# Optimization experiments

Hardware: AMD Instinct MI355X
Metric: run time of the kernel (lower is better)

## Reference

```python
import jax, jax.numpy as jnp
import numpy as np

FM = 128       # feature_maps
QM = 128       # query_maps
ROUNDS = 4     # test_rounds (training=False)
N_VARS = 24576
N_CLAUSES = 98304
N_EDGES = 3 * N_CLAUSES
EPS = 1e-6


def _dense(k, fan_in, fan_out):
    return jax.random.normal(k, (fan_in, fan_out), jnp.float32) * (1.0 / np.sqrt(fan_in))


def setup_inputs() -> dict:
    key = jax.random.key(0)
    ks = jax.random.split(key, 20)
    return {
        "edge_lit": jax.random.randint(ks[0], (N_EDGES,), 0, 2 * N_VARS, dtype=jnp.int32),
        "edge_clause": jnp.sort(jax.random.randint(ks[1], (N_EDGES,), 0, N_CLAUSES, dtype=jnp.int32)),
        "noise_v": jax.random.normal(ks[2], (ROUNDS, N_VARS, 4), jnp.float32),
        "noise_c": jax.random.normal(ks[3], (ROUNDS, N_CLAUSES, 4), jnp.float32),
        # variables_query: MLP(2, QM, QM), input FM+4
        "vq_w0": _dense(ks[4], FM + 4, QM), "vq_b0": jnp.zeros((QM,), jnp.float32),
        "vq_w1": _dense(ks[5], QM, QM),     "vq_b1": jnp.zeros((QM,), jnp.float32),
        # clauses_query: MLP(2, QM, QM), input FM+4
        "cq_w0": _dense(ks[6], FM + 4, QM), "cq_b0": jnp.zeros((QM,), jnp.float32),
        "cq_w1": _dense(ks[7], QM, QM),     "cq_b1": jnp.zeros((QM,), jnp.float32),
        # clause_update: MLP(2, 2*FM, FM+QM), input FM+2*QM=384
        "cm_w0": _dense(ks[8], FM + 2 * QM, 2 * FM), "cm_b0": jnp.zeros((2 * FM,), jnp.float32),
        "cm_w1": _dense(ks[9], 2 * FM, FM + QM),     "cm_b1": jnp.zeros((FM + QM,), jnp.float32),
        # update_gate: MLP(3, 2*FM, FM), input QM+FM+2*QM=512
        "ug_w0": _dense(ks[10], QM + FM + 2 * QM, 2 * FM), "ug_b0": jnp.zeros((2 * FM,), jnp.float32),
        "ug_w1": _dense(ks[11], 2 * FM, 2 * FM),           "ug_b1": jnp.zeros((2 * FM,), jnp.float32),
        "ug_w2": _dense(ks[12], 2 * FM, FM),               "ug_b2": jnp.zeros((FM,), jnp.float32),
        # clauses_mask_output: MLP(2, FM, 1)
        "co_w0": _dense(ks[13], FM, FM), "co_b0": jnp.zeros((FM,), jnp.float32),
        "co_w1": _dense(ks[14], FM, 1),  "co_b1": jnp.zeros((1,), jnp.float32),
        "n_vars": N_VARS,
        "n_clauses": N_CLAUSES,
    }


def _forward(edge_lit, edge_clause, n_vars, n_clauses, floats):
    (noise_v, noise_c,
     vq_w0, vq_b0, vq_w1, vq_b1,
     cq_w0, cq_b0, cq_w1, cq_b1,
     cm_w0, cm_b0, cm_w1, cm_b1,
     ug_w0, ug_b0, ug_w1, ug_b1, ug_w2, ug_b2,
     co_w0, co_b0, co_w1, co_b1) = floats

    n_edges = edge_lit.shape[0]
    # lit_degree = row sums of sparse adjacency (all nonzeros are 1.0)
    lit_degree = jax.ops.segment_sum(jnp.ones((n_edges,), jnp.float32), edge_lit,
                                     num_segments=2 * n_vars)[:, None]          # [2V,1]
    degree_weight = jax.lax.rsqrt(jnp.maximum(lit_degree, 1.0))
    var_degree_weight = 4.0 * jax.lax.rsqrt(
        jnp.maximum(lit_degree[:n_vars] + lit_degree[n_vars:], 1.0))            # [V,1]

    def mlp2(x, w0, b0, w1, b1):
        return jax.nn.relu(x @ w0 + b0) @ w1 + b1

    def mlp3(x, w0, b0, w1, b1, w2, b2):
        h = jax.nn.relu(x @ w0 + b0)
        h = jax.nn.relu(h @ w1 + b1)
        return h @ w2 + b2

    def pair_norm(x):
        # PairNorm(subtract_mean=True), single graph -> global mean over nodes
        x = x - jnp.mean(x, axis=0, keepdims=True)
        return x * jax.lax.rsqrt(jnp.mean(jnp.square(x)) + EPS)

    def clauses_loss_fn(vq, cq):
        # unsat_cnf_clauses_loss: softplus literal values aggregated per clause,
        # clause satisfiability exp(-sum), gated by clause query mask.
        lits = jax.nn.softplus(jnp.concatenate([vq, -vq], axis=0))              # [2V,Q]
        csum = jax.ops.segment_sum(lits[edge_lit], edge_clause,
                                   num_segments=n_clauses)                      # [C,Q]
        loss = jnp.exp(-csum) * jax.nn.sigmoid(cq)
        return jnp.mean(loss), loss

    grad_fn = jax.grad(clauses_loss_fn, argnums=(0, 1), has_aux=True)

    def step(carry, xs):
        variables, clauses = carry
        nv, nc = xs
        vq = mlp2(jnp.concatenate([variables, nv], -1), vq_w0, vq_b0, vq_w1, vq_b1)
        cq = mlp2(jnp.concatenate([clauses, nc], -1), cq_w0, cq_b0, cq_w1, cq_b1)
        (vgrad, cgrad), clauses_loss = grad_fn(vq, cq)
        vgrad = vgrad * var_degree_weight
        clauses_loss = clauses_loss * 4.0
        clause_data = mlp2(jnp.concatenate([clauses, clauses_loss, cgrad], -1),
                           cm_w0, cm_b0, cm_w1, cm_b1)                          # [C,FM+QM]
        variables_loss_all = clause_data[:, :QM]
        clauses = pair_norm(clause_data[:, QM:]) * 0.25 + 0.1 * clauses
        # adj_matrix @ variables_loss_all (literal-side aggregation)
        variables_loss = jax.ops.segment_sum(variables_loss_all[edge_clause], edge_lit,
                                             num_segments=2 * n_vars) * degree_weight
        unit = jnp.concatenate([vgrad, variables,
                                variables_loss[:n_vars], variables_loss[n_vars:]], -1)
        variables = pair_norm(mlp3(unit, ug_w0, ug_b0, ug_w1, ug_b1, ug_w2, ug_b2)) * 0.25 \
                    + 0.1 * variables
        logits = mlp2(clauses, co_w0, co_b0, co_w1, co_b1)[:, 0]                # [C]
        return (variables, clauses), logits

    init = (jnp.ones((n_vars, FM), jnp.float32), jnp.ones((n_clauses, FM), jnp.float32))
    _, logits = jax.lax.scan(step, init, (noise_v, noise_c))                    # [R,C]
    return jax.nn.sigmoid(logits), jax.nn.softplus(logits)


def reference(edge_lit, edge_clause, noise_v, noise_c,
              vq_w0, vq_b0, vq_w1, vq_b1,
              cq_w0, cq_b0, cq_w1, cq_b1,
              cm_w0, cm_b0, cm_w1, cm_b1,
              ug_w0, ug_b0, ug_w1, ug_b1, ug_w2, ug_b2,
              co_w0, co_b0, co_w1, co_b1,
              n_vars, n_clauses):
    floats = (noise_v, noise_c,
              vq_w0, vq_b0, vq_w1, vq_b1,
              cq_w0, cq_b0, cq_w1, cq_b1,
              cm_w0, cm_b0, cm_w1, cm_b1,
              ug_w0, ug_b0, ug_w1, ug_b1, ug_w2, ug_b2,
              co_w0, co_b0, co_w1, co_b1)
    return _forward(edge_lit, edge_clause, int(n_vars), int(n_clauses), floats)
```

## Files before the change

### kernel.cpp

```cpp
#include <hip/hip_runtime.h>
#include <math.h>

#define NV 24576
#define NC 98304
#define NE 294912
#define CMCHUNK 24576

typedef unsigned short bf16;
using bf8 = __attribute__((ext_vector_type(8))) short;
using f4  = __attribute__((ext_vector_type(4))) float;

static constexpr float INV_CQM = 1.0f / 12582912.0f;
static constexpr float LOG2E = 1.44269504f;
static constexpr float LN2 = 0.69314718f;

__device__ __forceinline__ float b2f(bf16 h) { return __uint_as_float(((unsigned)h) << 16); }
__device__ __forceinline__ bf16 f2b(float f) {
  unsigned u = __float_as_uint(f);
  u += 0x7fff + ((u >> 16) & 1);
  return (bf16)(u >> 16);
}
__device__ __forceinline__ float fexp2(float x) { float r; asm("v_exp_f32 %0, %1" : "=v"(r) : "v"(x)); return r; }
__device__ __forceinline__ float flog2(float x) { float r; asm("v_log_f32 %0, %1" : "=v"(r) : "v"(x)); return r; }
__device__ __forceinline__ float frcpf(float x) { float r; asm("v_rcp_f32 %0, %1" : "=v"(r) : "v"(x)); return r; }
__device__ __forceinline__ float fsigm(float x) { return frcpf(1.0f + fexp2(-x * LOG2E)); }
__device__ __forceinline__ float fsoftplus(float x) {
  return fmaxf(x, 0.0f) + LN2 * flog2(1.0f + fexp2(-fabsf(x) * LOG2E));
}
__device__ __forceinline__ float cvt_ld(float x) { return x; }
__device__ __forceinline__ float cvt_ld(bf16 x) { return b2f(x); }

__device__ __forceinline__ void gload16(const void* g, void* l) {
  __builtin_amdgcn_global_load_lds((const __attribute__((address_space(1))) unsigned int*)g,
                                   (__attribute__((address_space(3))) unsigned int*)l, 16, 0, 0);
}


__global__ __launch_bounds__(256) void k_cptr(const int* __restrict__ ec, int* __restrict__ ptr) {
  int c = blockIdx.x * 256 + threadIdx.x;
  if (c > NC) return;
  int lo = 0, hi = NE;
  while (lo < hi) { int mid = (lo + hi) >> 1; if (ec[mid] < c) lo = mid + 1; else hi = mid; }
  ptr[c] = lo;
}

__global__ __launch_bounds__(256) void k_litcnt(const int* __restrict__ el, int* __restrict__ cnt) {
  int e = blockIdx.x * 256 + threadIdx.x;
  atomicAdd(&cnt[el[e]], 1);
}

__global__ __launch_bounds__(1024) void k_scan(int* __restrict__ cnt, int* __restrict__ ptr) {
  __shared__ int wsum[16];
  __shared__ int carry_s;
  int tid = threadIdx.x, lane = tid & 63, w = tid >> 6;
  if (tid == 0) carry_s = 0;
  __syncthreads();
  for (int base = 0; base < 2 * NV; base += 1024) {
    int x = cnt[base + tid];
    int v = x;
#pragma unroll
    for (int off = 1; off < 64; off <<= 1) {
      int y = __shfl_up(v, off, 64);
      if (lane >= off) v += y;
    }
    if (lane == 63) wsum[w] = v;
    __syncthreads();
    int carry = carry_s;
    int wpre = 0;
    for (int i = 0; i < w; ++i) wpre += wsum[i];
    int excl = carry + wpre + (v - x);
    ptr[base + tid] = excl;
    cnt[base + tid] = excl;
    __syncthreads();
    if (tid == 1023) carry_s = carry + wpre + v;
  }
  __syncthreads();
  if (tid == 0) ptr[2 * NV] = carry_s;
}

__global__ __launch_bounds__(256) void k_fillsort(const int* __restrict__ el, const int* __restrict__ ec,
                                                  int* __restrict__ cur, int* __restrict__ lclause) {
  int e = blockIdx.x * 256 + threadIdx.x;
  int pos = atomicAdd(&cur[el[e]], 1);
  lclause[pos] = ec[e];
}

__global__ __launch_bounds__(256) void k_degree(const int* __restrict__ lptr, float* __restrict__ dw,
                                                float* __restrict__ vdw) {
  int l = blockIdx.x * 256 + threadIdx.x;
  if (l < 2 * NV) dw[l] = rsqrtf(fmaxf((float)(lptr[l + 1] - lptr[l]), 1.0f));
  if (l < NV) {
    int d = (lptr[l + 1] - lptr[l]) + (lptr[l + NV + 1] - lptr[l + NV]);
    vdw[l] = 4.0f * rsqrtf(fmaxf((float)d, 1.0f));
  }
}

__global__ __launch_bounds__(256) void k_init_v(float* __restrict__ variables, bf16* __restrict__ ugA) {
  int i = blockIdx.x * 256 + threadIdx.x;
  variables[i] = 1.0f;
  ugA[(size_t)(i >> 7) * 512 + 128 + (i & 127)] = 0x3F80;
}
__global__ __launch_bounds__(256) void k_init_c(bf16* __restrict__ cmA) {
  int i = blockIdx.x * 256 + threadIdx.x;
  cmA[(size_t)(i >> 7) * 384 + (i & 127)] = 0x3F80;
}

__global__ __launch_bounds__(256) void k_wt(const float* __restrict__ w, bf16* __restrict__ wt,
                                            int K, int N, int Kpad) {
  int idx = blockIdx.x * 256 + threadIdx.x;
  int n = idx / Kpad, k = idx % Kpad;
  if (n >= N) return;
  wt[idx] = (k < K) ? f2b(w[(size_t)k * N + n]) : (bf16)0;
}


template <bool CONCAT, bool RELU, int OUT>
__global__ __launch_bounds__(256) void mgemm(const bf16* __restrict__ A0, int lda,
                                             const float* __restrict__ noise,
                                             const bf16* __restrict__ WT,
                                             const float* __restrict__ Bv,
                                             void* out0, void* out1, int ldOut, int KDIM) {
  __shared__ __align__(16) char smem[32768];
  char* As = smem;
  char* Bs = smem + 16384;
  const int tid = threadIdx.x;
  const int m0 = blockIdx.x * 128;
  const int n0 = blockIdx.y * 128;
  const int lane = tid & 63;
  const int w = tid >> 6;
  const int wr = w >> 1, wc = w & 1;
  const int rl = (tid >> 3) & 7;
  const int cc = tid & 7;
  const int swzoff = (cc * 16) ^ (rl << 4);
  f4 acc[4][4] = {};
  for (int k0 = 0; k0 < KDIM; k0 += 64) {
    if (!CONCAT || k0 < 128) {
#pragma unroll
      for (int it = 0; it < 4; ++it) {
        int row0 = it * 32 + w * 8;
        int row = row0 + rl;
        gload16((const char*)(A0 + (size_t)(m0 + row) * lda + k0) + swzoff, As + row0 * 128);
        gload16((const char*)(WT + (size_t)(n0 + row) * KDIM + k0) + swzoff, Bs + row0 * 128);
      }
    } else {
      const int srow = tid >> 3, schunk = tid & 7;
#pragma unroll
      for (int it = 0; it < 4; ++it) {
        int row = srow + it * 32;
        alignas(16) bf16 tmp[8];
#pragma unroll
        for (int e = 0; e < 8; ++e) {
          int kk = schunk * 8 + e;
          tmp[e] = (kk < 4) ? f2b(noise[(size_t)(m0 + row) * 4 + kk]) : (bf16)0;
        }
        *reinterpret_cast<uint4*>(&As[row * 128 + ((schunk * 16) ^ ((row & 7) << 4))]) =
            *reinterpret_cast<uint4*>(tmp);
        int row0 = it * 32 + w * 8;
        gload16((const char*)(WT + (size_t)(n0 + row0 + rl) * KDIM + k0) + swzoff, Bs + row0 * 128);
      }
    }
    __syncthreads();
#pragma unroll
    for (int kk = 0; kk < 2; ++kk) {
      bf8 a[4], b[4];
#pragma unroll
      for (int i = 0; i < 4; ++i) {
        int r = wr * 64 + i * 16 + (lane & 15);
        int cby = (kk * 64 + ((lane >> 4) * 16)) ^ ((r & 7) << 4);
        a[i] = *reinterpret_cast<const bf8*>(&As[r * 128 + cby]);
        int c = wc * 64 + i * 16 + (lane & 15);
        int cby2 = (kk * 64 + ((lane >> 4) * 16)) ^ ((c & 7) << 4);
        b[i] = *reinterpret_cast<const bf8*>(&Bs[c * 128 + cby2]);
      }
#pragma unroll
      for (int i = 0; i < 4; ++i)
#pragma unroll
        for (int j = 0; j < 4; ++j)
          acc[i][j] = __builtin_amdgcn_mfma_f32_16x16x32_bf16(a[i], b[j], acc[i][j], 0, 0, 0);
    }
    __syncthreads();
  }
  const int colloc = wc * 64 + (lane & 15);
  const int rowbase = m0 + wr * 64 + ((lane >> 4) << 2);
#pragma unroll
  for (int j = 0; j < 4; ++j) {
    int c = n0 + colloc + j * 16;
    float bias = Bv[c];
#pragma unroll
    for (int i = 0; i < 4; ++i) {
      int rb = rowbase + i * 16;
#pragma unroll
      for (int p = 0; p < 4; ++p) {
        float v = acc[i][j][p] + bias;
        if (RELU) v = fmaxf(v, 0.0f);
        int r = rb + p;
        if constexpr (OUT == 0) {
          ((float*)out0)[(size_t)r * ldOut + c] = v;
        } else if constexpr (OUT == 1) {
          ((bf16*)out0)[(size_t)r * ldOut + c] = f2b(v);
        } else {
          bf16* o = (c < 128) ? (bf16*)out0 : (bf16*)out1;
          o[(size_t)r * 128 + (c & 127)] = f2b(v);
        }
      }
    }
  }
}


__global__ __launch_bounds__(256) void k_loss(const int* __restrict__ edge_lit, const int* __restrict__ cptr,
                                              const float* __restrict__ vq, const bf16* __restrict__ cq,
                                              bf16* __restrict__ cmA) {
  int c = blockIdx.x * 2 + (threadIdx.x >> 7);
  int q = threadIdx.x & 127;
  int e0 = cptr[c], e1 = cptr[c + 1];
  float csum = 0.0f;
  for (int e = e0; e < e1; ++e) {
    int lit = edge_lit[e];
    float x = (lit < NV) ? vq[(size_t)lit * 128 + q] : -vq[(size_t)(lit - NV) * 128 + q];
    csum += fsoftplus(x);
  }
  float s = fsigm(b2f(cq[(size_t)c * 128 + q]));
  float L = fexp2(-csum * LOG2E) * s;
  cmA[(size_t)c * 384 + 128 + q] = f2b(4.0f * L);
  cmA[(size_t)c * 384 + 256 + q] = f2b(L * (1.0f - s) * INV_CQM);
}

__global__ __launch_bounds__(256) void k_gather(const int* __restrict__ lptr, const int* __restrict__ lclause,
                                                const bf16* __restrict__ cmA, const bf16* __restrict__ cd0,
                                                bf16* __restrict__ gl, bf16* __restrict__ ugA,
                                                const float* __restrict__ dw) {
  int l = blockIdx.x * 2 + (threadIdx.x >> 7);
  int q = threadIdx.x & 127;
  int j0 = lptr[l], j1 = lptr[l + 1];
  float sg = 0.0f, sv = 0.0f;
  for (int j = j0; j < j1; ++j) {
    int c = lclause[j];
    sg += b2f(cmA[(size_t)c * 384 + 128 + q]);
    sv += b2f(cd0[(size_t)c * 128 + q]);
  }
  gl[(size_t)l * 128 + q] = f2b(sg);
  int r = (l < NV) ? l : l - NV;
  int cb = (l < NV) ? 256 : 384;
  ugA[(size_t)r * 512 + cb + q] = f2b(sv * dw[l]);
}

__global__ __launch_bounds__(256) void k_vgrad(const float* __restrict__ vq, const bf16* __restrict__ gl,
                                               const float* __restrict__ vdw, bf16* __restrict__ ugA) {
  int i = blockIdx.x * 256 + threadIdx.x;
  int v = i >> 7, q = i & 127;
  float s = fsigm(vq[i]);
  float gp = b2f(gl[(size_t)v * 128 + q]);
  float gn = b2f(gl[(size_t)(v + NV) * 128 + q]);
  float g = ((1.0f - s) * gn - s * gp) * (INV_CQM * 0.25f) * vdw[v];
  ugA[(size_t)v * 512 + q] = f2b(g);
}

template <typename T>
__global__ __launch_bounds__(256) void k_pn_stats(const T* __restrict__ X, int R, float* __restrict__ stats) {
  int q = threadIdx.x & 127;
  int rg = threadIdx.x >> 7;
  float cs = 0.0f, ss = 0.0f;
  for (int r = blockIdx.x * 2 + rg; r < R; r += gridDim.x * 2) {
    float x = cvt_ld(X[(size_t)r * 128 + q]);
    cs += x;
    ss += x * x;
  }
  __shared__ float scs[256], sss[256];
  scs[threadIdx.x] = cs;
  sss[threadIdx.x] = ss;
  __syncthreads();
  if (threadIdx.x < 128) atomicAdd(&stats[q], scs[q] + scs[128 + q]);
  for (int off = 128; off; off >>= 1) {
    if (threadIdx.x < off) sss[threadIdx.x] += sss[threadIdx.x + off];
    __syncthreads();
  }
  if (threadIdx.x == 0) atomicAdd(&stats[128], sss[0]);
}

__global__ __launch_bounds__(128) void k_pn_final(float* __restrict__ stats, float R) {
  __shared__ float s[128];
  int q = threadIdx.x;
  float m = stats[q] / R;
  s[q] = m * m;
  __syncthreads();
  for (int off = 64; off; off >>= 1) {
    if (q < off) s[q] += s[q + off];
    __syncthreads();
  }
  if (q == 0) {
    float var = (stats[128] - R * s[0]) / (R * 128.0f);
    stats[129] = rsqrtf(fmaxf(var, 0.0f) + 1e-6f) * 0.25f;
  }
  stats[q] = m;
}

__global__ __launch_bounds__(256) void k_pn_apply_c(const bf16* __restrict__ cd1, const float* __restrict__ stats,
                                                    bf16* __restrict__ cmA) {
  int i = blockIdx.x * 256 + threadIdx.x;
  int c = i >> 7, q = i & 127;
  float x = b2f(cd1[i]);
  float old = b2f(cmA[(size_t)c * 384 + q]);
  cmA[(size_t)c * 384 + q] = f2b((x - stats[q]) * stats[129] + 0.1f * old);
}

__global__ __launch_bounds__(256) void k_pn_apply_v(const float* __restrict__ uout, const float* __restrict__ stats,
                                                    float* __restrict__ variables, bf16* __restrict__ ugA) {
  int i = blockIdx.x * 256 + threadIdx.x;
  int v = i >> 7, q = i & 127;
  float nv = (uout[i] - stats[q]) * stats[129] + 0.1f * variables[i];
  variables[i] = nv;
  ugA[(size_t)v * 512 + 128 + q] = f2b(nv);
}

__global__ __launch_bounds__(256) void k_logits(const bf16* __restrict__ lh, const float* __restrict__ w1,
                                                const float* __restrict__ b1, float* __restrict__ outp, int t) {
  int wv = threadIdx.x >> 6, lane = threadIdx.x & 63;
  int c = blockIdx.x * 4 + wv;
  const bf16* row = lh + (size_t)c * 128;
  float v = b2f(row[lane]) * w1[lane] + b2f(row[64 + lane]) * w1[64 + lane];
#pragma unroll
  for (int off = 32; off; off >>= 1) v += __shfl_down(v, off, 64);
  if (lane == 0) {
    float lg = v + b1[0];
    outp[(size_t)t * NC + c] = fsigm(lg);
    outp[(size_t)4 * NC + (size_t)t * NC + c] = fsoftplus(lg);
  }
}


extern "C" void kernel_launch(void* const* d_in, const int* in_sizes, int n_in,
                              void* d_out, int out_size, void* d_ws, size_t ws_size,
                              hipStream_t stream) {
  const int* edge_lit = (const int*)d_in[0];
  const int* edge_clause = (const int*)d_in[1];
  const float* noise_v = (const float*)d_in[2];
  const float* noise_c = (const float*)d_in[3];
  const float* vq_w0 = (const float*)d_in[4];  const float* vq_b0 = (const float*)d_in[5];
  const float* vq_w1 = (const float*)d_in[6];  const float* vq_b1 = (const float*)d_in[7];
  const float* cq_w0 = (const float*)d_in[8];  const float* cq_b0 = (const float*)d_in[9];
  const float* cq_w1 = (const float*)d_in[10]; const float* cq_b1 = (const float*)d_in[11];
  const float* cm_w0 = (const float*)d_in[12]; const float* cm_b0 = (const float*)d_in[13];
  const float* cm_w1 = (const float*)d_in[14]; const float* cm_b1 = (const float*)d_in[15];
  const float* ug_w0 = (const float*)d_in[16]; const float* ug_b0 = (const float*)d_in[17];
  const float* ug_w1 = (const float*)d_in[18]; const float* ug_b1 = (const float*)d_in[19];
  const float* ug_w2 = (const float*)d_in[20]; const float* ug_b2 = (const float*)d_in[21];
  const float* co_w0 = (const float*)d_in[22]; const float* co_b0 = (const float*)d_in[23];
  const float* co_w1 = (const float*)d_in[24]; const float* co_b1 = (const float*)d_in[25];
  float* out = (float*)d_out;

  char* base = (char*)d_ws;
  size_t off = 0;
  auto A = [&](size_t n) -> char* {
    char* p = base + off;
    off = (off + n + 255) & ~(size_t)255;
    return p;
  };
  float* variables = (float*)A((size_t)NV * 128 * 4);
  float* vq        = (float*)A((size_t)NV * 128 * 4);
  bf16* cmA        = (bf16*)A((size_t)NC * 384 * 2);
  bf16* ugA        = (bf16*)A((size_t)NV * 512 * 2);
  char* R_cq       = A((size_t)NC * 128 * 2);
  char* R_h        = A((size_t)NC * 128 * 2);
  char* R_big      = A((size_t)2 * NV * 128 * 2 + (size_t)NV * 128 * 4);
  bf16* wtb        = (bf16*)A(983424);
  int* cptr = (int*)A((size_t)(NC + 1) * 4);
  int* lptr = (int*)A((size_t)(2 * NV + 1) * 4);
  int* lcur = (int*)A((size_t)2 * NV * 4);
  int* lclause = (int*)A((size_t)NE * 4);
  float* dw  = (float*)A((size_t)2 * NV * 4);
  float* vdw = (float*)A((size_t)NV * 4);
  float* stats = (float*)A(2048);
  if (off > ws_size) {
    hipMemsetAsync(d_out, 0xFF, (size_t)out_size * 4, stream);
    return;
  }

  bf16* cq  = (bf16*)R_cq;
  bf16* cd0 = (bf16*)R_cq;
  bf16* lh  = (bf16*)R_cq;
  bf16* hv  = (bf16*)R_h;
  bf16* hc  = (bf16*)R_h;
  bf16* cd1 = (bf16*)R_h;
  bf16* uh1 = (bf16*)R_h;
  bf16* uh2 = (bf16*)(R_h + (size_t)NV * 256 * 2);
  bf16* cmh = (bf16*)R_big;
  bf16* gl  = (bf16*)R_big;
  float* uout = (float*)(R_big + (size_t)2 * NV * 128 * 2);

  size_t wo = 0;
  auto WTa = [&](int n, int kp) { bf16* p = wtb + wo; wo += (size_t)n * kp; return p; };
  bf16* wt_vq0 = WTa(128, 192); bf16* wt_vq1 = WTa(128, 128);
  bf16* wt_cq0 = WTa(128, 192); bf16* wt_cq1 = WTa(128, 128);
  bf16* wt_cm0 = WTa(256, 384); bf16* wt_cm1 = WTa(256, 256);
  bf16* wt_ug0 = WTa(256, 512); bf16* wt_ug1 = WTa(256, 256);
  bf16* wt_ug2 = WTa(128, 256); bf16* wt_co0 = WTa(128, 128);

  hipMemsetAsync(lcur, 0, (size_t)2 * NV * 4, stream);
  k_cptr<<<(NC + 256) / 256, 256, 0, stream>>>(edge_clause, cptr);
  k_litcnt<<<NE / 256, 256, 0, stream>>>(edge_lit, lcur);
  k_scan<<<1, 1024, 0, stream>>>(lcur, lptr);
  k_fillsort<<<NE / 256, 256, 0, stream>>>(edge_lit, edge_clause, lcur, lclause);
  k_degree<<<(2 * NV + 255) / 256, 256, 0, stream>>>(lptr, dw, vdw);
  k_init_v<<<NV * 128 / 256, 256, 0, stream>>>(variables, ugA);
  k_init_c<<<NC * 128 / 256, 256, 0, stream>>>(cmA);
  k_wt<<<128 * 192 / 256, 256, 0, stream>>>(vq_w0, wt_vq0, 132, 128, 192);
  k_wt<<<128 * 128 / 256, 256, 0, stream>>>(vq_w1, wt_vq1, 128, 128, 128);
  k_wt<<<128 * 192 / 256, 256, 0, stream>>>(cq_w0, wt_cq0, 132, 128, 192);
  k_wt<<<128 * 128 / 256, 256, 0, stream>>>(cq_w1, wt_cq1, 128, 128, 128);
  k_wt<<<256 * 384 / 256, 256, 0, stream>>>(cm_w0, wt_cm0, 384, 256, 384);
  k_wt<<<256 * 256 / 256, 256, 0, stream>>>(cm_w1, wt_cm1, 256, 256, 256);
  k_wt<<<256 * 512 / 256, 256, 0, stream>>>(ug_w0, wt_ug0, 512, 256, 512);
  k_wt<<<256 * 256 / 256, 256, 0, stream>>>(ug_w1, wt_ug1, 256, 256, 256);
  k_wt<<<128 * 256 / 256, 256, 0, stream>>>(ug_w2, wt_ug2, 256, 128, 256);
  k_wt<<<128 * 128 / 256, 256, 0, stream>>>(co_w0, wt_co0, 128, 128, 128);

  for (int t = 0; t < 4; ++t) {
    const float* nvp = noise_v + (size_t)t * NV * 4;
    const float* ncp = noise_c + (size_t)t * NC * 4;
    mgemm<true, true, 1><<<dim3(NV / 128, 1), 256, 0, stream>>>(ugA + 128, 512, nvp, wt_vq0, vq_b0, hv, nullptr, 128, 192);
    mgemm<false, false, 0><<<dim3(NV / 128, 1), 256, 0, stream>>>(hv, 128, nullptr, wt_vq1, vq_b1, vq, nullptr, 128, 128);
    mgemm<true, true, 1><<<dim3(NC / 128, 1), 256, 0, stream>>>(cmA, 384, ncp, wt_cq0, cq_b0, hc, nullptr, 128, 192);
    mgemm<false, false, 1><<<dim3(NC / 128, 1), 256, 0, stream>>>(hc, 128, nullptr, wt_cq1, cq_b1, cq, nullptr, 128, 128);
    k_loss<<<NC / 2, 256, 0, stream>>>(edge_lit, cptr, vq, cq, cmA);
    for (int ch = 0; ch < NC / CMCHUNK; ++ch) {
      size_t ro = (size_t)ch * CMCHUNK;
      mgemm<false, true, 1><<<dim3(CMCHUNK / 128, 2), 256, 0, stream>>>(cmA + ro * 384, 384, nullptr, wt_cm0, cm_b0, cmh, nullptr, 256, 384);
      mgemm<false, false, 2><<<dim3(CMCHUNK / 128, 2), 256, 0, stream>>>(cmh, 256, nullptr, wt_cm1, cm_b1, cd0 + ro * 128, cd1 + ro * 128, 128, 256);
    }
    k_gather<<<NV, 256, 0, stream>>>(lptr, lclause, cmA, cd0, gl, ugA, dw);
    k_vgrad<<<NV * 128 / 256, 256, 0, stream>>>(vq, gl, vdw, ugA);
    hipMemsetAsync(stats, 0, 132 * 4, stream);
    k_pn_stats<bf16><<<256, 256, 0, stream>>>(cd1, NC, stats);
    k_pn_final<<<1, 128, 0, stream>>>(stats, (float)NC);
    k_pn_apply_c<<<NC * 128 / 256, 256, 0, stream>>>(cd1, stats, cmA);
    mgemm<false, true, 1><<<dim3(NC / 128, 1), 256, 0, stream>>>(cmA, 384, nullptr, wt_co0, co_b0, lh, nullptr, 128, 128);
    k_logits<<<NC / 4, 256, 0, stream>>>(lh, co_w1, co_b1, out, t);
    mgemm<false, true, 1><<<dim3(NV / 128, 2), 256, 0, stream>>>(ugA, 512, nullptr, wt_ug0, ug_b0, uh1, nullptr, 256, 512);
    mgemm<false, true, 1><<<dim3(NV / 128, 2), 256, 0, stream>>>(uh1, 256, nullptr, wt_ug1, ug_b1, uh2, nullptr, 256, 256);
    mgemm<false, false, 0><<<dim3(NV / 128, 1), 256, 0, stream>>>(uh2, 256, nullptr, wt_ug2, ug_b2, uout, nullptr, 128, 256);
    hipMemsetAsync(stats, 0, 132 * 4, stream);
    k_pn_stats<float><<<256, 256, 0, stream>>>(uout, NV, stats);
    k_pn_final<<<1, 128, 0, stream>>>(stats, (float)NV);
    k_pn_apply_v<<<NV * 128 / 256, 256, 0, stream>>>(uout, stats, variables, ugA);
  }
}
```

Measured before the change: 2.104 ms.

## Double-buffer GEMM loads, precompute fp16 softplus tables, fuse gather with vgrad

```diff
diff --git a/kernel.cpp b/kernel.cpp
--- a/kernel.cpp
+++ b/kernel.cpp
@@ -7,6 +7,7 @@
 #define CMCHUNK 24576
 
 typedef unsigned short bf16;
+typedef _Float16 f16;
 using bf8 = __attribute__((ext_vector_type(8))) short;
 using f4  = __attribute__((ext_vector_type(4))) float;
 
@@ -114,15 +115,14 @@
 }
 
 
-template <bool CONCAT, bool RELU, int OUT>
+template <int KDIM, bool CONCAT, bool RELU, int OUT>
 __global__ __launch_bounds__(256) void mgemm(const bf16* __restrict__ A0, int lda,
                                              const float* __restrict__ noise,
                                              const bf16* __restrict__ WT,
                                              const float* __restrict__ Bv,
-                                             void* out0, void* out1, int ldOut, int KDIM) {
-  __shared__ __align__(16) char smem[32768];
-  char* As = smem;
-  char* Bs = smem + 16384;
+                                             void* out0, void* out1, int ldOut) {
+  __shared__ __align__(16) char smem[65536];
+  constexpr int NT = KDIM / 64;
   const int tid = threadIdx.x;
   const int m0 = blockIdx.x * 128;
   const int n0 = blockIdx.y * 128;
@@ -132,8 +132,11 @@
   const int rl = (tid >> 3) & 7;
   const int cc = tid & 7;
   const int swzoff = (cc * 16) ^ (rl << 4);
-  f4 acc[4][4] = {};
-  for (int k0 = 0; k0 < KDIM; k0 += 64) {
+
+  auto stage = [&](int t, int buf) {
+    char* As = smem + buf * 32768;
+    char* Bs = As + 16384;
+    const int k0 = t * 64;
     if (!CONCAT || k0 < 128) {
 #pragma unroll
       for (int it = 0; it < 4; ++it) {
@@ -159,7 +162,28 @@
         gload16((const char*)(WT + (size_t)(n0 + row0 + rl) * KDIM + k0) + swzoff, Bs + row0 * 128);
       }
     }
-    __syncthreads();
+  };
+
+  f4 acc[4][4] = {};
+  stage(0, 0);
+#pragma unroll
+  for (int t = 0; t < NT; ++t) {
+    const int buf = t & 1;
+    __builtin_amdgcn_sched_barrier(0);
+    if (t + 1 < NT) {
+      stage(t + 1, buf ^ 1);
+      if (CONCAT && (t + 1) * 64 >= 128) {
+        asm volatile("s_waitcnt vmcnt(4) lgkmcnt(0)" ::: "memory");
+      } else {
+        asm volatile("s_waitcnt vmcnt(8) lgkmcnt(0)" ::: "memory");
+      }
+    } else {
+      asm volatile("s_waitcnt vmcnt(0) lgkmcnt(0)" ::: "memory");
+    }
+    __builtin_amdgcn_s_barrier();
+    __builtin_amdgcn_sched_barrier(0);
+    const char* As = smem + buf * 32768;
+    const char* Bs = As + 16384;
 #pragma unroll
     for (int kk = 0; kk < 2; ++kk) {
       bf8 a[4], b[4];
@@ -178,7 +202,8 @@
         for (int j = 0; j < 4; ++j)
           acc[i][j] = __builtin_amdgcn_mfma_f32_16x16x32_bf16(a[i], b[j], acc[i][j], 0, 0, 0);
     }
-    __syncthreads();
+    __builtin_amdgcn_sched_barrier(0);
+    __builtin_amdgcn_s_barrier();
   }
   const int colloc = wc * 64 + (lane & 15);
   const int rowbase = m0 + wr * 64 + ((lane >> 4) << 2);
@@ -198,9 +223,13 @@
           ((float*)out0)[(size_t)r * ldOut + c] = v;
         } else if constexpr (OUT == 1) {
           ((bf16*)out0)[(size_t)r * ldOut + c] = f2b(v);
-        } else {
+        } else if constexpr (OUT == 2) {
           bf16* o = (c < 128) ? (bf16*)out0 : (bf16*)out1;
           o[(size_t)r * 128 + (c & 127)] = f2b(v);
+        } else {
+          float tq = LN2 * flog2(1.0f + fexp2(-fabsf(v) * LOG2E));
+          ((f16*)out0)[(size_t)r * 128 + c] = (f16)(fmaxf(v, 0.0f) + tq);
+          ((f16*)out1)[(size_t)r * 128 + c] = (f16)(fmaxf(-v, 0.0f) + tq);
         }
       }
     }
@@ -209,16 +238,16 @@
 
 
 __global__ __launch_bounds__(256) void k_loss(const int* __restrict__ edge_lit, const int* __restrict__ cptr,
-                                              const float* __restrict__ vq, const bf16* __restrict__ cq,
-                                              bf16* __restrict__ cmA) {
+                                              const f16* __restrict__ spp, const f16* __restrict__ spn,
+                                              const bf16* __restrict__ cq, bf16* __restrict__ cmA) {
   int c = blockIdx.x * 2 + (threadIdx.x >> 7);
   int q = threadIdx.x & 127;
   int e0 = cptr[c], e1 = cptr[c + 1];
   float csum = 0.0f;
   for (int e = e0; e < e1; ++e) {
     int lit = edge_lit[e];
-    float x = (lit < NV) ? vq[(size_t)lit * 128 + q] : -vq[(size_t)(lit - NV) * 128 + q];
-    csum += fsoftplus(x);
+    const f16* base = (lit < NV) ? (spp + (size_t)lit * 128) : (spn + (size_t)(lit - NV) * 128);
+    csum += (float)base[q];
   }
   float s = fsigm(b2f(cq[(size_t)c * 128 + q]));
   float L = fexp2(-csum * LOG2E) * s;
@@ -226,12 +255,13 @@
   cmA[(size_t)c * 384 + 256 + q] = f2b(L * (1.0f - s) * INV_CQM);
 }
 
-__global__ __launch_bounds__(256) void k_gather(const int* __restrict__ lptr, const int* __restrict__ lclause,
-                                                const bf16* __restrict__ cmA, const bf16* __restrict__ cd0,
-                                                bf16* __restrict__ gl, bf16* __restrict__ ugA,
-                                                const float* __restrict__ dw) {
-  int l = blockIdx.x * 2 + (threadIdx.x >> 7);
-  int q = threadIdx.x & 127;
+__global__ __launch_bounds__(256) void k_gatherv(const int* __restrict__ lptr, const int* __restrict__ lclause,
+                                                 const bf16* __restrict__ cmA, const bf16* __restrict__ cd0,
+                                                 const f16* __restrict__ spn, const float* __restrict__ dw,
+                                                 const float* __restrict__ vdw, bf16* __restrict__ ugA) {
+  int v = blockIdx.x;
+  int half = threadIdx.x >> 7, q = threadIdx.x & 127;
+  int l = v + half * NV;
   int j0 = lptr[l], j1 = lptr[l + 1];
   float sg = 0.0f, sv = 0.0f;
   for (int j = j0; j < j1; ++j) {
@@ -239,21 +269,15 @@
     sg += b2f(cmA[(size_t)c * 384 + 128 + q]);
     sv += b2f(cd0[(size_t)c * 128 + q]);
   }
-  gl[(size_t)l * 128 + q] = f2b(sg);
-  int r = (l < NV) ? l : l - NV;
-  int cb = (l < NV) ? 256 : 384;
-  ugA[(size_t)r * 512 + cb + q] = f2b(sv * dw[l]);
-}
-
-__global__ __launch_bounds__(256) void k_vgrad(const float* __restrict__ vq, const bf16* __restrict__ gl,
-                                               const float* __restrict__ vdw, bf16* __restrict__ ugA) {
-  int i = blockIdx.x * 256 + threadIdx.x;
-  int v = i >> 7, q = i & 127;
-  float s = fsigm(vq[i]);
-  float gp = b2f(gl[(size_t)v * 128 + q]);
-  float gn = b2f(gl[(size_t)(v + NV) * 128 + q]);
-  float g = ((1.0f - s) * gn - s * gp) * (INV_CQM * 0.25f) * vdw[v];
-  ugA[(size_t)v * 512 + q] = f2b(g);
+  __shared__ float sgl[2][128];
+  sgl[half][q] = sg;
+  ugA[(size_t)v * 512 + 256 + half * 128 + q] = f2b(sv * dw[l]);
+  __syncthreads();
+  if (half == 0) {
+    float s = fexp2(-LOG2E * (float)spn[(size_t)v * 128 + q]);
+    float g = ((1.0f - s) * sgl[1][q] - s * sgl[0][q]) * (INV_CQM * 0.25f) * vdw[v];
+    ugA[(size_t)v * 512 + q] = f2b(g);
+  }
 }
 
 template <typename T>
@@ -357,7 +381,6 @@
     return p;
   };
   float* variables = (float*)A((size_t)NV * 128 * 4);
-  float* vq        = (float*)A((size_t)NV * 128 * 4);
   bf16* cmA        = (bf16*)A((size_t)NC * 384 * 2);
   bf16* ugA        = (bf16*)A((size_t)NV * 512 * 2);
   char* R_cq       = A((size_t)NC * 128 * 2);
@@ -385,8 +408,9 @@
   bf16* uh1 = (bf16*)R_h;
   bf16* uh2 = (bf16*)(R_h + (size_t)NV * 256 * 2);
   bf16* cmh = (bf16*)R_big;
-  bf16* gl  = (bf16*)R_big;
-  float* uout = (float*)(R_big + (size_t)2 * NV * 128 * 2);
+  f16* spp  = (f16*)(R_big + 12582912);
+  f16* spn  = spp + (size_t)NV * 128;
+  float* uout = (float*)(R_big + 12582912);
 
   size_t wo = 0;
   auto WTa = [&](int n, int kp) { bf16* p = wtb + wo; wo += (size_t)n * kp; return p; };
@@ -418,27 +442,26 @@
   for (int t = 0; t < 4; ++t) {
     const float* nvp = noise_v + (size_t)t * NV * 4;
     const float* ncp = noise_c + (size_t)t * NC * 4;
-    mgemm<true, true, 1><<<dim3(NV / 128, 1), 256, 0, stream>>>(ugA + 128, 512, nvp, wt_vq0, vq_b0, hv, nullptr, 128, 192);
-    mgemm<false, false, 0><<<dim3(NV / 128, 1), 256, 0, stream>>>(hv, 128, nullptr, wt_vq1, vq_b1, vq, nullptr, 128, 128);
-    mgemm<true, true, 1><<<dim3(NC / 128, 1), 256, 0, stream>>>(cmA, 384, ncp, wt_cq0, cq_b0, hc, nullptr, 128, 192);
-    mgemm<false, false, 1><<<dim3(NC / 128, 1), 256, 0, stream>>>(hc, 128, nullptr, wt_cq1, cq_b1, cq, nullptr, 128, 128);
-    k_loss<<<NC / 2, 256, 0, stream>>>(edge_lit, cptr, vq, cq, cmA);
+    mgemm<192, true, true, 1><<<dim3(NV / 128, 1), 256, 0, stream>>>(ugA + 128, 512, nvp, wt_vq0, vq_b0, hv, nullptr, 128);
+    mgemm<128, false, false, 3><<<dim3(NV / 128, 1), 256, 0, stream>>>(hv, 128, nullptr, wt_vq1, vq_b1, spp, spn, 128);
+    mgemm<192, true, true, 1><<<dim3(NC / 128, 1), 256, 0, stream>>>(cmA, 384, ncp, wt_cq0, cq_b0, hc, nullptr, 128);
+    mgemm<128, false, false, 1><<<dim3(NC / 128, 1), 256, 0, stream>>>(hc, 128, nullptr, wt_cq1, cq_b1, cq, nullptr, 128);
+    k_loss<<<NC / 2, 256, 0, stream>>>(edge_lit, cptr, spp, spn, cq, cmA);
     for (int ch = 0; ch < NC / CMCHUNK; ++ch) {
       size_t ro = (size_t)ch * CMCHUNK;
-      mgemm<false, true, 1><<<dim3(CMCHUNK / 128, 2), 256, 0, stream>>>(cmA + ro * 384, 384, nullptr, wt_cm0, cm_b0, cmh, nullptr, 256, 384);
-      mgemm<false, false, 2><<<dim3(CMCHUNK / 128, 2), 256, 0, stream>>>(cmh, 256, nullptr, wt_cm1, cm_b1, cd0 + ro * 128, cd1 + ro * 128, 128, 256);
-    }
-    k_gather<<<NV, 256, 0, stream>>>(lptr, lclause, cmA, cd0, gl, ugA, dw);
-    k_vgrad<<<NV * 128 / 256, 256, 0, stream>>>(vq, gl, vdw, ugA);
+      mgemm<384, false, true, 1><<<dim3(CMCHUNK / 128, 2), 256, 0, stream>>>(cmA + ro * 384, 384, nullptr, wt_cm0, cm_b0, cmh, nullptr, 256);
+      mgemm<256, false, false, 2><<<dim3(CMCHUNK / 128, 2), 256, 0, stream>>>(cmh, 256, nullptr, wt_cm1, cm_b1, cd0 + ro * 128, cd1 + ro * 128, 128);
+    }
+    k_gatherv<<<NV, 256, 0, stream>>>(lptr, lclause, cmA, cd0, spn, dw, vdw, ugA);
     hipMemsetAsync(stats, 0, 132 * 4, stream);
     k_pn_stats<bf16><<<256, 256, 0, stream>>>(cd1, NC, stats);
     k_pn_final<<<1, 128, 0, stream>>>(stats, (float)NC);
     k_pn_apply_c<<<NC * 128 / 256, 256, 0, stream>>>(cd1, stats, cmA);
-    mgemm<false, true, 1><<<dim3(NC / 128, 1), 256, 0, stream>>>(cmA, 384, nullptr, wt_co0, co_b0, lh, nullptr, 128, 128);
+    mgemm<128, false, true, 1><<<dim3(NC / 128, 1), 256, 0, stream>>>(cmA, 384, nullptr, wt_co0, co_b0, lh, nullptr, 128);
     k_logits<<<NC / 4, 256, 0, stream>>>(lh, co_w1, co_b1, out, t);
-    mgemm<false, true, 1><<<dim3(NV / 128, 2), 256, 0, stream>>>(ugA, 512, nullptr, wt_ug0, ug_b0, uh1, nullptr, 256, 512);
-    mgemm<false, true, 1><<<dim3(NV / 128, 2), 256, 0, stream>>>(uh1, 256, nullptr, wt_ug1, ug_b1, uh2, nullptr, 256, 256);
-    mgemm<false, false, 0><<<dim3(NV / 128, 1), 256, 0, stream>>>(uh2, 256, nullptr, wt_ug2, ug_b2, uout, nullptr, 128, 256);
+    mgemm<512, false, true, 1><<<dim3(NV / 128, 2), 256, 0, stream>>>(ugA, 512, nullptr, wt_ug0, ug_b0, uh1, nullptr, 256);
+    mgemm<256, false, true, 1><<<dim3(NV / 128, 2), 256, 0, stream>>>(uh1, 256, nullptr, wt_ug1, ug_b1, uh2, nullptr, 256);
+    mgemm<256, false, false, 0><<<dim3(NV / 128, 1), 256, 0, stream>>>(uh2, 256, nullptr, wt_ug2, ug_b2, uout, nullptr, 128);
     hipMemsetAsync(stats, 0, 132 * 4, stream);
     k_pn_stats<float><<<256, 256, 0, stream>>>(uout, NV, stats);
     k_pn_final<<<1, 128, 0, stream>>>(stats, (float)NV);
```

Result: faster. 1.988 ms (-5.5%).
